# Kernel optimization log

Measured on AMD Instinct MI355X. Metric: run time of the kernel, lower is better.

The kernel has to match this reference:

```python
import jax, jax.numpy as jnp
import numpy as np

D_MODEL = 1152
NUM_HEADS = 16
HEAD_DIM = D_MODEL // NUM_HEADS
B, N, M = 8, 4096, 300


def setup_inputs() -> dict:
    key = jax.random.key(0)
    ks = jax.random.split(key, 10)
    s = 0.02
    x = jax.random.normal(ks[0], (B, N, D_MODEL), dtype=jnp.float32)
    cond = jax.random.normal(ks[1], (B, M, D_MODEL), dtype=jnp.float32)
    # per-sample valid conditioning lengths in [1, M]
    mask = jax.random.randint(ks[2], (B,), 1, M + 1, dtype=jnp.int32)
    wq = jax.random.normal(ks[3], (D_MODEL, D_MODEL), dtype=jnp.float32) * s
    bq = jnp.zeros((D_MODEL,), dtype=jnp.float32)
    wkv = jax.random.normal(ks[4], (D_MODEL, 2 * D_MODEL), dtype=jnp.float32) * s
    bkv = jnp.zeros((2 * D_MODEL,), dtype=jnp.float32)
    wp = jax.random.normal(ks[5], (D_MODEL, D_MODEL), dtype=jnp.float32) * s
    bp = jnp.zeros((D_MODEL,), dtype=jnp.float32)
    return {"x": x, "cond": cond, "mask": mask, "wq": wq, "bq": bq,
            "wkv": wkv, "bkv": bkv, "wp": wp, "bp": bp}


def reference(x, cond, mask, wq, bq, wkv, bkv, wp, bp):
    b, n, c = x.shape
    m = cond.shape[1]
    # projections
    q = (x @ wq + bq).reshape(b, n, NUM_HEADS, HEAD_DIM)
    kv = (cond @ wkv + bkv).reshape(b, m, 2, NUM_HEADS, HEAD_DIM)
    k, v = kv[:, :, 0], kv[:, :, 1]
    scale = 1.0 / jnp.sqrt(jnp.asarray(HEAD_DIM, dtype=x.dtype))
    # [b, h, n, m] attention scores
    scores = jnp.einsum("bnhd,bmhd->bhnm", q, k) * scale
    # key positions j < mask[i] are valid (matches torch bool attn_mask)
    valid = (jnp.arange(m)[None, :] < mask[:, None])  # [b, m]
    bias = jnp.where(valid, 0.0, -1e9).astype(scores.dtype)[:, None, None, :]
    attn = jax.nn.softmax(scores + bias, axis=-1)
    out = jnp.einsum("bhnm,bmhd->bnhd", attn, v).reshape(b, n, c)
    return out @ wp + bp
```

## Files before the change

### kernel.cpp

```cpp
#include <hip/hip_runtime.h>
#include <cstdint>

typedef unsigned short u16;
typedef __attribute__((ext_vector_type(8))) short short8;
typedef __attribute__((ext_vector_type(4))) float floatx4;

#define BAR()      __builtin_amdgcn_s_barrier()
#define SCHEDBAR() __builtin_amdgcn_sched_barrier(0)

__device__ __forceinline__ u16 f2bf(float f) {
    unsigned u = __float_as_uint(f);
    u += 0x7FFFu + ((u >> 16) & 1u);
    return (u16)(u >> 16);
}

__device__ __forceinline__ void async16(const void* g, void* l) {
    __builtin_amdgcn_global_load_lds(
        (const __attribute__((address_space(1))) unsigned*)g,
        (__attribute__((address_space(3))) unsigned*)l, 16, 0, 0);
}

__global__ void cast_bf16_kernel(const float* __restrict__ in, u16* __restrict__ out, long n8) {
    long i = (long)blockIdx.x * 256 + threadIdx.x;
    if (i >= n8) return;
    const float4* p = (const float4*)in;
    float4 a = p[i * 2], b = p[i * 2 + 1];
    uint4 o;
    o.x = f2bf(a.x) | ((unsigned)f2bf(a.y) << 16);
    o.y = f2bf(a.z) | ((unsigned)f2bf(a.w) << 16);
    o.z = f2bf(b.x) | ((unsigned)f2bf(b.y) << 16);
    o.w = f2bf(b.z) | ((unsigned)f2bf(b.w) << 16);
    ((uint4*)out)[i] = o;
}

__global__ void fill_zero(uint4* __restrict__ p, int n) {
    int i = blockIdx.x * 256 + threadIdx.x;
    if (i < n) p[i] = (uint4){0u, 0u, 0u, 0u};
}

__global__ void transpose_cast(const float* __restrict__ W, u16* __restrict__ Wt, int K, int N) {
    __shared__ float tile[32][33];
    int bx = blockIdx.x * 32, by = blockIdx.y * 32;
    int tx = threadIdx.x, ty = threadIdx.y;
#pragma unroll
    for (int i = 0; i < 32; i += 8)
        tile[ty + i][tx] = W[(long)(by + ty + i) * N + bx + tx];
    __syncthreads();
#pragma unroll
    for (int i = 0; i < 32; i += 8)
        Wt[(long)(bx + ty + i) * K + by + tx] = f2bf(tile[tx][ty + i]);
}

__device__ __forceinline__ void rd8(short8 (&a)[2][4], const u16* sm, int base, int g0, int g1) {
#pragma unroll
    for (int mi = 0; mi < 4; ++mi) {
        a[0][mi] = *(const short8*)&sm[base + mi * 1024 + g0];
        a[1][mi] = *(const short8*)&sm[base + mi * 1024 + g1];
    }
}
__device__ __forceinline__ void rd6(short8 (&b)[2][3], const u16* sm, int base, int g0, int g1) {
#pragma unroll
    for (int ni = 0; ni < 3; ++ni) {
        b[0][ni] = *(const short8*)&sm[base + ni * 1024 + g0];
        b[1][ni] = *(const short8*)&sm[base + ni * 1024 + g1];
    }
}
__device__ __forceinline__ void mfma24(floatx4 (&ah)[4][3], const short8 (&a)[2][4], const short8 (&b)[2][3]) {
#pragma unroll
    for (int kk = 0; kk < 2; ++kk)
#pragma unroll
        for (int mi = 0; mi < 4; ++mi)
#pragma unroll
            for (int ni = 0; ni < 3; ++ni)
                ah[mi][ni] = __builtin_amdgcn_mfma_f32_16x16x32_bf16(a[kk][mi], b[kk][ni], ah[mi][ni], 0, 0, 0);
}

template <int MODE>
__global__ __launch_bounds__(512, 2)
void gemm8p(const u16* __restrict__ A, const u16* __restrict__ Bt,
            const float* __restrict__ bias, float scale,
            u16* __restrict__ outA, float* __restrict__ outF) {
    extern __shared__ u16 smem[];
    const int K = 1152;
    const int tid = threadIdx.x, lane = tid & 63, wave = tid >> 6;
    const int quad = lane >> 4, cl = lane & 15;
    const int wm = wave >> 2, wn = wave & 3;
    const int l3 = lane >> 3, l7 = lane & 7;
    const int w8 = wave * 8;

    int bid = blockIdx.x;
    int swz = (bid & 7) * 96 + (bid >> 3);
    int colTile = swz % 6, rowTile = swz / 6;
    const long rowBase = (long)rowTile * 256;
    const int colBase = colTile * 192;

    const int sg = (l7 ^ l3) * 8;
    const u16* pA = A + (rowBase + l3) * (long)K + sg;
    const u16* pB = Bt + ((long)colBase + l3) * (long)K + sg;

    auto stA = [&](int Ts, int r0) {
        async16(pA + (long)r0 * K + Ts * 64, &smem[(Ts & 1) * 16384 + r0 * 64]);
    };
    auto stB = [&](int Ts, int r0) {
        async16(pB + (long)r0 * K + Ts * 64, &smem[32768 + (Ts & 1) * 12288 + r0 * 64]);
    };

    const int arow = wm * 8192 + cl * 64;
    const int brow = wn * 3072 + cl * 64;
    const int gs0 = (quad ^ (cl & 7)) * 8;
    const int gs1 = ((4 + quad) ^ (cl & 7)) * 8;

    floatx4 acc[2][4][3];
#pragma unroll
    for (int h = 0; h < 2; ++h)
#pragma unroll
        for (int i = 0; i < 4; ++i)
#pragma unroll
            for (int j = 0; j < 3; ++j) acc[h][i][j] = (floatx4){0.f, 0.f, 0.f, 0.f};

    short8 a0[2][4], a1[2][4], bf[2][3];

    stA(0, w8); stA(0, 128 + w8);
    stB(0, w8); stB(0, 64 + w8); stB(0, 128 + w8);
    stA(0, 64 + w8); stA(0, 192 + w8);
    stA(1, w8); stA(1, 128 + w8);
    stB(1, w8); stB(1, 64 + w8); stB(1, 128 + w8);
    SCHEDBAR();
    asm volatile("s_waitcnt vmcnt(7)");
    SCHEDBAR();
    BAR();

#pragma unroll 2
    for (int T = 0; T < 16; ++T) {
        const int ab = (T & 1) * 16384;
        const int bb = 32768 + (T & 1) * 12288;
        rd8(a0, smem, ab + arow, gs0, gs1);
        rd6(bf, smem, bb + brow, gs0, gs1);
        stA(T + 1, 64 + w8); stA(T + 1, 192 + w8);
        SCHEDBAR(); BAR();
        asm volatile("s_waitcnt lgkmcnt(0)"); SCHEDBAR();
        __builtin_amdgcn_s_setprio(1);
        mfma24(acc[0], a0, bf);
        __builtin_amdgcn_s_setprio(0);
        SCHEDBAR();
        asm volatile("s_waitcnt vmcnt(7)"); SCHEDBAR(); BAR();
        rd8(a1, smem, ab + arow + 4096, gs0, gs1);
        stA(T + 2, w8); stA(T + 2, 128 + w8);
        stB(T + 2, w8); stB(T + 2, 64 + w8); stB(T + 2, 128 + w8);
        SCHEDBAR(); BAR();
        asm volatile("s_waitcnt lgkmcnt(0)"); SCHEDBAR();
        __builtin_amdgcn_s_setprio(1);
        mfma24(acc[1], a1, bf);
        __builtin_amdgcn_s_setprio(0);
        SCHEDBAR();
        asm volatile("s_waitcnt vmcnt(7)"); SCHEDBAR(); BAR();
    }

    {
        const int ab = 0, bb = 32768;
        rd8(a0, smem, ab + arow, gs0, gs1);
        rd6(bf, smem, bb + brow, gs0, gs1);
        stA(17, 64 + w8); stA(17, 192 + w8);
        SCHEDBAR(); BAR();
        asm volatile("s_waitcnt lgkmcnt(0)"); SCHEDBAR();
        __builtin_amdgcn_s_setprio(1);
        mfma24(acc[0], a0, bf);
        __builtin_amdgcn_s_setprio(0);
        SCHEDBAR();
        asm volatile("s_waitcnt vmcnt(7)"); SCHEDBAR(); BAR();
        rd8(a1, smem, ab + arow + 4096, gs0, gs1);
        SCHEDBAR(); BAR();
        asm volatile("s_waitcnt lgkmcnt(0)"); SCHEDBAR();
        __builtin_amdgcn_s_setprio(1);
        mfma24(acc[1], a1, bf);
        __builtin_amdgcn_s_setprio(0);
        SCHEDBAR();
        asm volatile("s_waitcnt vmcnt(2)"); SCHEDBAR(); BAR();
    }
    {
        const int ab = 16384, bb = 32768 + 12288;
        rd8(a0, smem, ab + arow, gs0, gs1);
        rd6(bf, smem, bb + brow, gs0, gs1);
        SCHEDBAR(); BAR();
        asm volatile("s_waitcnt lgkmcnt(0)"); SCHEDBAR();
        __builtin_amdgcn_s_setprio(1);
        mfma24(acc[0], a0, bf);
        __builtin_amdgcn_s_setprio(0);
        SCHEDBAR();
        asm volatile("s_waitcnt vmcnt(0)"); SCHEDBAR(); BAR();
        rd8(a1, smem, ab + arow + 4096, gs0, gs1);
        SCHEDBAR();
        asm volatile("s_waitcnt lgkmcnt(0)"); SCHEDBAR();
        __builtin_amdgcn_s_setprio(1);
        mfma24(acc[1], a1, bf);
        __builtin_amdgcn_s_setprio(0);
        SCHEDBAR();
    }

#pragma unroll
    for (int h = 0; h < 2; ++h)
#pragma unroll
        for (int mi = 0; mi < 4; ++mi) {
            long row = rowBase + wm * 128 + (h * 4 + mi) * 16 + quad * 4;
#pragma unroll
            for (int ni = 0; ni < 3; ++ni) {
                int col = colBase + wn * 48 + ni * 16 + cl;
                float bv = bias[col];
#pragma unroll
                for (int r = 0; r < 4; ++r) {
                    float v = (acc[h][mi][ni][r] + bv) * scale;
                    if (MODE == 0) outA[(row + r) * 1152 + col] = f2bf(v);
                    else           outF[(row + r) * 1152L + col] = v;
                }
            }
        }
}

template <int MODE>
__global__ __launch_bounds__(256)
void gemm_bt(const u16* __restrict__ A, const u16* __restrict__ Bt,
             const float* __restrict__ bias, float scale,
             u16* __restrict__ outA, u16* __restrict__ outB, float* __restrict__ outF,
             int M, int N, int K) {
    __shared__ u16 As[128 * 32];
    __shared__ u16 Bs[128 * 32];
    const int tid = threadIdx.x, lane = tid & 63, wave = tid >> 6;
    const int wm = wave >> 1, wn = wave & 1;
    const int quad = lane >> 4, cl = lane & 15;
    const long rowBase = (long)blockIdx.x * 128;
    const int colBase = blockIdx.y * 128;
    const int srow = lane >> 2;
    const int skc = (lane & 3) * 8;

    floatx4 acc[4][4];
#pragma unroll
    for (int i = 0; i < 4; i++)
#pragma unroll
        for (int j = 0; j < 4; j++) acc[i][j] = (floatx4){0.f, 0.f, 0.f, 0.f};

    for (int k0 = 0; k0 < K; k0 += 32) {
#pragma unroll
        for (int j = 0; j < 2; ++j) {
            int inst = wave * 2 + j;
            long r = rowBase + inst * 16 + srow;
            if (r > (long)M - 1) r = (long)M - 1;
            async16(A + r * K + k0 + skc, &As[inst * 512]);
        }
#pragma unroll
        for (int j = 0; j < 2; ++j) {
            int inst = wave * 2 + j;
            long r = colBase + inst * 16 + srow;
            async16(Bt + r * K + k0 + skc, &Bs[inst * 512]);
        }
        __syncthreads();
        short8 af[4], bfr[4];
#pragma unroll
        for (int mi = 0; mi < 4; mi++)
            af[mi] = *(const short8*)&As[(wm * 64 + mi * 16 + cl) * 32 + quad * 8];
#pragma unroll
        for (int ni = 0; ni < 4; ni++)
            bfr[ni] = *(const short8*)&Bs[(wn * 64 + ni * 16 + cl) * 32 + quad * 8];
#pragma unroll
        for (int mi = 0; mi < 4; mi++)
#pragma unroll
            for (int ni = 0; ni < 4; ni++)
                acc[mi][ni] = __builtin_amdgcn_mfma_f32_16x16x32_bf16(af[mi], bfr[ni], acc[mi][ni], 0, 0, 0);
        __syncthreads();
    }

#pragma unroll
    for (int mi = 0; mi < 4; mi++) {
        long row0 = rowBase + wm * 64 + mi * 16 + quad * 4;
#pragma unroll
        for (int ni = 0; ni < 4; ni++) {
            int col = colBase + wn * 64 + ni * 16 + cl;
            float bv = bias[col];
#pragma unroll
            for (int r = 0; r < 4; r++) {
                long row = row0 + r;
                if (row < M) {
                    float v = (acc[mi][ni][r] + bv) * scale;
                    if (MODE == 1) {
                        int bb = (int)(row / 300);
                        int mm = (int)(row - (long)bb * 300);
                        if (col < 1152) {
                            int hh = col / 72, dd = col - hh * 72;
                            outA[((long)(bb * 16 + hh) * 384 + mm) * 72 + dd] = f2bf(v);
                        } else {
                            int c2 = col - 1152;
                            int hh = c2 / 72, dd = c2 - hh * 72;
                            int ch = mm >> 7, mc = mm & 127;
                            int g = (mc >> 3) ^ (dd & 7);
                            outB[(((long)(bb * 16 + hh) * 3 + ch) * 72 + dd) * 128 + g * 8 + (mc & 7)] = f2bf(v);
                        }
                    }
                }
            }
        }
    }
}

__global__ __launch_bounds__(256, 4)
void attn_kernel(const u16* __restrict__ Q, const u16* __restrict__ K,
                 const u16* __restrict__ V, const int* __restrict__ mask,
                 u16* __restrict__ O) {
    __shared__ __align__(16) u16 smem[(18432 + 20480) / 2];
    u16* Ks = smem;
    u16* Vs = smem + 9216;

    const int tid = threadIdx.x, lane = tid & 63, wave = tid >> 6;
    const int quad = lane >> 4, cl = lane & 15;
    const int b = blockIdx.z, h = blockIdx.y, nt = blockIdx.x;
    int mb = mask[b];
    if (mb > 300) mb = 300;
    if (mb < 1) mb = 1;
    const int bh = b * 16 + h;

    const long qbase = ((long)b * 4096 + nt * 64) * 1152 + h * 72;

    const u16* qrow = Q + qbase + (long)(wave * 16 + cl) * 1152;
    short8 zero8 = {0, 0, 0, 0, 0, 0, 0, 0};
    short8 aq[3];
    aq[0] = *(const short8*)(qrow + quad * 8);
    aq[1] = *(const short8*)(qrow + 32 + quad * 8);
    aq[2] = (quad == 0) ? *(const short8*)(qrow + 64) : zero8;

    if (tid < 16) {
        unsigned fill = 0x3F803F80u;
        *(uint4*)&Vs[72 * 128 + tid * 8] = (uint4){fill, fill, fill, fill};
    }

    floatx4 oacc[5];
#pragma unroll
    for (int i = 0; i < 5; i++) oacc[i] = (floatx4){0.f, 0.f, 0.f, 0.f};

    const u16* kb = K + (long)bh * 384 * 72;
    const u16* vb = V + (long)bh * 3 * 9216;

    const int nch = (mb + 127) >> 7;
    for (int ch = 0; ch < nch; ++ch) {
        const int base = ch << 7;
        __syncthreads();

        const u16* ksrc = kb + (long)base * 72;
        for (int i = wave; i < 18; i += 4)
            async16(ksrc + i * 512 + lane * 8, Ks + i * 512);
        const u16* vsrc = vb + (long)ch * 9216;
        for (int i = wave; i < 18; i += 4)
            async16(vsrc + i * 512 + lane * 8, Vs + i * 512);
        __syncthreads();

        floatx4 sacc[8];
#pragma unroll
        for (int t = 0; t < 8; t++) sacc[t] = (floatx4){0.f, 0.f, 0.f, 0.f};
#pragma unroll
        for (int kk = 0; kk < 3; ++kk) {
#pragma unroll
            for (int t = 0; t < 8; ++t) {
                short8 bfr = *(const short8*)&Ks[(t * 16 + cl) * 72 + kk * 32 + quad * 8];
                sacc[t] = __builtin_amdgcn_mfma_f32_16x16x32_bf16(aq[kk], bfr, sacc[t], 0, 0, 0);
            }
        }
        __syncthreads();

#pragma unroll
        for (int r = 0; r < 4; ++r) {
            int prow = (wave * 16 + quad * 4 + r) * 136;
#pragma unroll
            for (int t = 0; t < 8; ++t) {
                int col = base + t * 16 + cl;
                float p = (col < mb) ? __expf(sacc[t][r]) : 0.f;
                unsigned pb = f2bf(p);
                unsigned ob = __shfl_xor(pb, 1);
                if (!(lane & 1))
                    *(unsigned*)&Ks[prow + t * 16 + cl] = pb | (ob << 16);
            }
        }

#pragma unroll
        for (int kk = 0; kk < 4; ++kk) {
            short8 pf = *(const short8*)&Ks[(wave * 16 + cl) * 136 + kk * 32 + quad * 8];
#pragma unroll
            for (int dt = 0; dt < 5; ++dt) {
                int dd = dt * 16 + cl;
                short8 vf = *(const short8*)&Vs[dd * 128 + (((kk * 4 + quad) ^ (dd & 7)) << 3)];
                oacc[dt] = __builtin_amdgcn_mfma_f32_16x16x32_bf16(pf, vf, oacc[dt], 0, 0, 0);
            }
        }
    }

#pragma unroll
    for (int r = 0; r < 4; r++) {
        float l = __shfl(oacc[4][r], (lane & 48) + 8);
        float inv = 1.0f / l;
        int row = wave * 16 + quad * 4 + r;
#pragma unroll
        for (int dt = 0; dt < 5; dt++) {
            int dd = dt * 16 + cl;
            if (dd < 72) O[qbase + (long)row * 1152 + dd] = f2bf(oacc[dt][r] * inv);
        }
    }
}

extern "C" void kernel_launch(void* const* d_in, const int* in_sizes, int n_in,
                              void* d_out, int out_size, void* d_ws, size_t ws_size,
                              hipStream_t stream) {
    const float* x    = (const float*)d_in[0];
    const float* cond = (const float*)d_in[1];
    const int*   mask = (const int*)d_in[2];
    const float* wq   = (const float*)d_in[3];
    const float* bq   = (const float*)d_in[4];
    const float* wkv  = (const float*)d_in[5];
    const float* bkv  = (const float*)d_in[6];
    const float* wp   = (const float*)d_in[7];
    const float* bp   = (const float*)d_in[8];

    char* ws = (char*)d_ws;
    u16* xb    = (u16*)(ws);
    u16* condb = (u16*)(ws + 75497472ll);
    u16* wkvT  = (u16*)(ws + 81027072ll);
    u16* qbuf  = (u16*)(ws + 86335488ll);
    u16* kbuf  = (u16*)(ws + 161832960ll);
    u16* vbuf  = (u16*)(ws + 168910848ll);
    u16* wqT   = (u16*)(ws + 161832960ll);
    u16* wpT   = (u16*)(ws + 161832960ll);
    if (ws_size < 175988736ull) return;

    static bool s_attr = false;
    if (!s_attr) {
        hipFuncSetAttribute((const void*)gemm8p<0>, hipFuncAttributeMaxDynamicSharedMemorySize, 114688);
        hipFuncSetAttribute((const void*)gemm8p<2>, hipFuncAttributeMaxDynamicSharedMemorySize, 114688);
        s_attr = true;
    }

    cast_bf16_kernel<<<18432, 256, 0, stream>>>(x, xb, 4718592ll);
    cast_bf16_kernel<<<1350, 256, 0, stream>>>(cond, condb, 345600ll);

    transpose_cast<<<dim3(36, 36), dim3(32, 8), 0, stream>>>(wq, wqT, 1152, 1152);
    transpose_cast<<<dim3(72, 36), dim3(32, 8), 0, stream>>>(wkv, wkvT, 1152, 2304);

    gemm8p<0><<<768, 512, 114688, stream>>>(xb, wqT, bq, 0.11785113019775793f, qbuf, nullptr);

    fill_zero<<<3456, 256, 0, stream>>>((uint4*)kbuf, 884736);
    gemm_bt<1><<<dim3(19, 18), 256, 0, stream>>>(condb, wkvT, bkv, 1.0f,
                                                 kbuf, vbuf, nullptr, 2400, 2304, 1152);
    attn_kernel<<<dim3(64, 16, 8), 256, 0, stream>>>(qbuf, kbuf, vbuf, mask, xb);

    transpose_cast<<<dim3(36, 36), dim3(32, 8), 0, stream>>>(wp, wpT, 1152, 1152);
    gemm8p<2><<<768, 512, 114688, stream>>>(xb, wpT, bp, 1.0f, nullptr, (float*)d_out);
}
```

Baseline: 616.8 us.

## Swizzle K layout to 128-wide rows and skip masked key tiles in attention

The KV projection now writes K into an XOR-swizzled 128-element row layout, and the attention kernel reads K and the P tile with a matching swizzle to avoid LDS bank conflicts. K loads, QK^T MFMAs, softmax writes and PV MFMAs are limited to the key tiles that fall inside the valid mask length, so work on padded keys is skipped. The shared-memory footprint grows, occupancy drops from 4 to 3 blocks, and the inner loops are no longer fully unrolled. The attention output is written in place over the Q buffer and the workspace is re-laid out to match.

```diff
diff --git a/kernel.cpp b/kernel.cpp
--- a/kernel.cpp
+++ b/kernel.cpp
@@ -285,7 +285,8 @@
                         int mm = (int)(row - (long)bb * 300);
                         if (col < 1152) {
                             int hh = col / 72, dd = col - hh * 72;
-                            outA[((long)(bb * 16 + hh) * 384 + mm) * 72 + dd] = f2bf(v);
+                            int pg = (dd >> 3) ^ (mm & 7);
+                            outA[((long)(bb * 16 + hh) * 384 + mm) * 128 + pg * 8 + (dd & 7)] = f2bf(v);
                         } else {
                             int c2 = col - 1152;
                             int hh = c2 / 72, dd = c2 - hh * 72;
@@ -300,13 +301,13 @@
     }
 }
 
-__global__ __launch_bounds__(256, 4)
+__global__ __launch_bounds__(256, 3)
 void attn_kernel(const u16* __restrict__ Q, const u16* __restrict__ K,
                  const u16* __restrict__ V, const int* __restrict__ mask,
                  u16* __restrict__ O) {
-    __shared__ __align__(16) u16 smem[(18432 + 20480) / 2];
+    __shared__ __align__(16) u16 smem[(32768 + 20480) / 2];
     u16* Ks = smem;
-    u16* Vs = smem + 9216;
+    u16* Vs = smem + 16384;
 
     const int tid = threadIdx.x, lane = tid & 63, wave = tid >> 6;
     const int quad = lane >> 4, cl = lane & 15;
@@ -334,16 +335,20 @@
 #pragma unroll
     for (int i = 0; i < 5; i++) oacc[i] = (floatx4){0.f, 0.f, 0.f, 0.f};
 
-    const u16* kb = K + (long)bh * 384 * 72;
+    const u16* kb = K + (long)bh * 384 * 128;
     const u16* vb = V + (long)bh * 3 * 9216;
 
+    const int xr = (cl & 7);
     const int nch = (mb + 127) >> 7;
     for (int ch = 0; ch < nch; ++ch) {
         const int base = ch << 7;
+        const int rem = mb - base;
+        const int kklim = (rem + 31) >> 5 > 4 ? 4 : (rem + 31) >> 5;
+        const int tlim = kklim * 2;
         __syncthreads();
 
-        const u16* ksrc = kb + (long)base * 72;
-        for (int i = wave; i < 18; i += 4)
+        const u16* ksrc = kb + (long)base * 128;
+        for (int i = wave; i < 4 * tlim; i += 4)
             async16(ksrc + i * 512 + lane * 8, Ks + i * 512);
         const u16* vsrc = vb + (long)ch * 9216;
         for (int i = wave; i < 18; i += 4)
@@ -353,11 +358,10 @@
         floatx4 sacc[8];
 #pragma unroll
         for (int t = 0; t < 8; t++) sacc[t] = (floatx4){0.f, 0.f, 0.f, 0.f};
-#pragma unroll
         for (int kk = 0; kk < 3; ++kk) {
-#pragma unroll
-            for (int t = 0; t < 8; ++t) {
-                short8 bfr = *(const short8*)&Ks[(t * 16 + cl) * 72 + kk * 32 + quad * 8];
+            const int pg = ((kk * 4 + quad) ^ xr) * 8;
+            for (int t = 0; t < tlim; ++t) {
+                short8 bfr = *(const short8*)&Ks[(t * 16 + cl) * 128 + pg];
                 sacc[t] = __builtin_amdgcn_mfma_f32_16x16x32_bf16(aq[kk], bfr, sacc[t], 0, 0, 0);
             }
         }
@@ -365,21 +369,24 @@
 
 #pragma unroll
         for (int r = 0; r < 4; ++r) {
-            int prow = (wave * 16 + quad * 4 + r) * 136;
-#pragma unroll
-            for (int t = 0; t < 8; ++t) {
+            int prow = wave * 16 + quad * 4 + r;
+            int pb8 = prow * 128 + (cl & 6);
+            int rk = (prow & 7);
+            for (int t = 0; t < tlim; ++t) {
                 int col = base + t * 16 + cl;
                 float p = (col < mb) ? __expf(sacc[t][r]) : 0.f;
-                unsigned pb = f2bf(p);
-                unsigned ob = __shfl_xor(pb, 1);
-                if (!(lane & 1))
-                    *(unsigned*)&Ks[prow + t * 16 + cl] = pb | (ob << 16);
+                float po = __shfl_xor(p, 1);
+                if (!(lane & 1)) {
+                    unsigned pk;
+                    asm("v_cvt_pk_bf16_f32 %0, %1, %2" : "=v"(pk) : "v"(p), "v"(po));
+                    int pg = ((t * 2 + (cl >> 3)) ^ rk) * 8;
+                    *(unsigned*)&Ks[pb8 + pg] = pk;
+                }
             }
         }
 
-#pragma unroll
-        for (int kk = 0; kk < 4; ++kk) {
-            short8 pf = *(const short8*)&Ks[(wave * 16 + cl) * 136 + kk * 32 + quad * 8];
+        for (int kk = 0; kk < kklim; ++kk) {
+            short8 pf = *(const short8*)&Ks[(wave * 16 + cl) * 128 + ((kk * 4 + quad) ^ xr) * 8];
 #pragma unroll
             for (int dt = 0; dt < 5; ++dt) {
                 int dd = dt * 16 + cl;
@@ -417,11 +424,11 @@
 
     char* ws = (char*)d_ws;
     u16* xb    = (u16*)(ws);
-    u16* condb = (u16*)(ws + 75497472ll);
-    u16* wkvT  = (u16*)(ws + 81027072ll);
-    u16* qbuf  = (u16*)(ws + 86335488ll);
-    u16* kbuf  = (u16*)(ws + 161832960ll);
-    u16* vbuf  = (u16*)(ws + 168910848ll);
+    u16* kswz  = (u16*)(ws);
+    u16* vbuf  = (u16*)(ws + 12582912ll);
+    u16* qbuf  = (u16*)(ws + 75497472ll);
+    u16* condb = (u16*)(ws + 150994944ll);
+    u16* wkvT  = (u16*)(ws + 156524544ll);
     u16* wqT   = (u16*)(ws + 161832960ll);
     u16* wpT   = (u16*)(ws + 161832960ll);
     if (ws_size < 175988736ull) return;
@@ -441,11 +448,11 @@
 
     gemm8p<0><<<768, 512, 114688, stream>>>(xb, wqT, bq, 0.11785113019775793f, qbuf, nullptr);
 
-    fill_zero<<<3456, 256, 0, stream>>>((uint4*)kbuf, 884736);
+    fill_zero<<<4800, 256, 0, stream>>>((uint4*)kswz, 1228800);
     gemm_bt<1><<<dim3(19, 18), 256, 0, stream>>>(condb, wkvT, bkv, 1.0f,
-                                                 kbuf, vbuf, nullptr, 2400, 2304, 1152);
-    attn_kernel<<<dim3(64, 16, 8), 256, 0, stream>>>(qbuf, kbuf, vbuf, mask, xb);
+                                                 kswz, vbuf, nullptr, 2400, 2304, 1152);
+    attn_kernel<<<dim3(64, 16, 8), 256, 0, stream>>>(qbuf, kswz, vbuf, mask, qbuf);
 
     transpose_cast<<<dim3(36, 36), dim3(32, 8), 0, stream>>>(wp, wpT, 1152, 1152);
-    gemm8p<2><<<768, 512, 114688, stream>>>(xb, wpT, bp, 1.0f, nullptr, (float*)d_out);
-}
+    gemm8p<2><<<768, 512, 114688, stream>>>(qbuf, wpT, bp, 1.0f, nullptr, (float*)d_out);
+}
```

New measurement: 621.1 us. Within noise of the previous version (+0.7%).
